# Performance work log

Hardware: AMD Instinct MI355X
Metric: run time of the kernel (lower is better)

The kernel has to match this reference:

```python
import jax, jax.numpy as jnp
import numpy as np

B, N, K, D, H, FF, L, NH = 8, 50, 20, 3, 128, 2048, 3, 8
S = N * K
HD = H // NH


def setup_inputs() -> dict:
    key = jax.random.key(0)
    ks = jax.random.split(key, 16)
    visited = jax.random.uniform(ks[0], (B, S)) < 0.05
    # the single most-recent action per batch row (status flips 0 -> 1)
    action_idx = jax.random.randint(ks[1], (B,), 0, S)
    visited = visited.at[jnp.arange(B), action_idx].set(True)
    feats = jax.random.normal(ks[2], (B, S, D - 1)) * visited[:, :, None]
    state = jnp.concatenate([feats, visited[:, :, None].astype(jnp.float32)], axis=-1)
    prev_state = state.at[jnp.arange(B), action_idx, :].set(0.0)

    def w(k, shape, s=0.02):
        return jax.random.normal(k, shape, dtype=jnp.float32) * s

    return dict(
        prev_state=prev_state, state=state,
        W_pre=w(ks[3], (D, H)), b_pre=jnp.zeros(H),
        Wq=w(ks[4], (L, H, H)), bq=jnp.zeros((L, H)),
        Wk=w(ks[5], (L, H, H)), bk=jnp.zeros((L, H)),
        Wv=w(ks[6], (L, H, H)), bv=jnp.zeros((L, H)),
        Wo=w(ks[7], (L, H, H)), bo=jnp.zeros((L, H)),
        ln1_g=jnp.ones((L, H)), ln1_b=jnp.zeros((L, H)),
        Wff1=w(ks[8], (L, H, FF)), bff1=jnp.zeros((L, FF)),
        Wff2=w(ks[9], (L, FF, H)), bff2=jnp.zeros((L, H)),
        ln2_g=jnp.ones((L, H)), ln2_b=jnp.zeros((L, H)),
        W_comb=w(ks[10], (2 * H, H)), b_comb=jnp.zeros(H),
        W_dec=w(ks[11], (H, H)), b_dec=jnp.zeros(H),
        W_lin=w(ks[12], (S, S)), b_lin=jnp.zeros(S),
    )


def _layer_norm(x, g, b, eps=1e-5):
    m = jnp.mean(x, -1, keepdims=True)
    v = jnp.mean(jnp.square(x - m), -1, keepdims=True)
    return (x - m) * jax.lax.rsqrt(v + eps) * g + b


def _update_mask(state):
    # vectorized equivalent of the original Python-loop scatter mask
    status = state[:, :, -1] != 0                      # visited [B, S], S = K*N channel-major
    mask = status
    vis_kn = status.reshape(B, K, N)
    user_any = vis_kn.any(axis=1)                      # [B, N]: user visited on any channel
    mask = mask | jnp.broadcast_to(user_any[:, None, :], (B, K, N)).reshape(B, S)
    assigned = state.reshape(B, K, N, D).sum(-1) != 0  # [B, K, N]
    full = assigned.sum(-1) >= 2                       # [B, K]: channel already has 2 users
    mask = mask | jnp.broadcast_to(full[:, :, None], (B, K, N)).reshape(B, S)
    return mask


def reference(prev_state, state, W_pre, b_pre, Wq, bq, Wk, bk, Wv, bv, Wo, bo,
              ln1_g, ln1_b, Wff1, bff1, Wff2, bff2, ln2_g, ln2_b,
              W_comb, b_comb, W_dec, b_dec, W_lin, b_lin):
    mask = _update_mask(state)
    # exactly one status change per batch row (sequential RL step)
    diff = prev_state[:, :, -1] != state[:, :, -1]
    act_idx = jnp.argmax(diff, axis=1)                 # [B]

    x = state @ W_pre + b_pre                          # [B, S, H]
    scale = np.float32(1.0 / np.sqrt(HD))
    for i in range(L):  # 3 post-LN transformer encoder layers
        q = (x @ Wq[i] + bq[i]).reshape(B, S, NH, HD)
        k = (x @ Wk[i] + bk[i]).reshape(B, S, NH, HD)
        v = (x @ Wv[i] + bv[i]).reshape(B, S, NH, HD)
        att = jax.nn.softmax(jnp.einsum('bqhd,bkhd->bhqk', q, k) * scale, axis=-1)
        o = jnp.einsum('bhqk,bkhd->bqhd', att, v).reshape(B, S, H) @ Wo[i] + bo[i]
        x = _layer_norm(x + o, ln1_g[i], ln1_b[i])
        ff = jax.nn.relu(x @ Wff1[i] + bff1[i]) @ Wff2[i] + bff2[i]
        x = _layer_norm(x + ff, ln2_g[i], ln2_b[i])

    last = x[jnp.arange(B), act_idx]                   # [B, H]
    combined = jnp.concatenate([x.mean(axis=1), last], axis=-1)  # [B, 2H]
    g = combined @ W_comb + b_comb                     # [B, H]
    dec = x @ W_dec + b_dec                            # [B, S, H]
    scores = jnp.einsum('bsh,bh->bs', dec, g)          # [B, S]
    masked = scores @ W_lin + b_lin                    # Q-Learning head
    return jnp.where(mask, -jnp.inf, masked)
```

## Files before the change

### kernel.cpp

```cpp
#include <hip/hip_runtime.h>
#include <math.h>

#define Bb 8
#define Ss 1000
#define Kk 20
#define Nn 50
#define Dd 3
#define Hh 128
#define FFf 2048
#define Ll 3
#define NHh 8
#define HDd 16
#define ROWS (Bb*Ss)

#define SENTINEL -3.0e38f

typedef unsigned short ush;
typedef short short8 __attribute__((ext_vector_type(8)));
typedef float f32x4 __attribute__((ext_vector_type(4)));

__device__ __forceinline__ ush f2b(float f) {
  unsigned x = __float_as_uint(f);
  return (ush)((x + 0x7fff + ((x >> 16) & 1)) >> 16);
}

__global__ __launch_bounds__(256) void mask_kernel(const float* __restrict__ state,
                                                   const float* __restrict__ prev_state,
                                                   int* __restrict__ mask, int* __restrict__ act_idx) {
  int b = blockIdx.x, tid = threadIdx.x;
  __shared__ unsigned char status[Ss], assigned[Ss], uany[Nn], fullk[Kk];
  __shared__ int act;
  if (tid == 0) act = 1 << 30;
  __syncthreads();
  for (int s = tid; s < Ss; s += 256) {
    const float* st = state + ((size_t)b * Ss + s) * Dd;
    float f2 = st[2];
    status[s] = (f2 != 0.f);
    assigned[s] = ((st[0] + st[1] + f2) != 0.f);
    float p2 = prev_state[((size_t)b * Ss + s) * Dd + 2];
    if (p2 != f2) atomicMin(&act, s);
  }
  __syncthreads();
  if (tid < Nn) {
    unsigned char a = 0;
    for (int k = 0; k < Kk; ++k) a |= status[k * Nn + tid];
    uany[tid] = a;
  } else if (tid >= 64 && tid < 64 + Kk) {
    int k = tid - 64, cnt = 0;
    for (int n = 0; n < Nn; ++n) cnt += assigned[k * Nn + n];
    fullk[k] = (cnt >= 2);
  }
  __syncthreads();
  for (int s = tid; s < Ss; s += 256)
    mask[b * Ss + s] = (int)(status[s] | uany[s % Nn] | fullk[s / Nn]);
  if (tid == 0) act_idx[b] = (act >= Ss) ? 0 : act;
}

__global__ __launch_bounds__(256) void pre_kernel(const float* __restrict__ state,
                                                  const float* __restrict__ W_pre,
                                                  const float* __restrict__ b_pre,
                                                  float* __restrict__ x, ush* __restrict__ xbf) {
  int idx = blockIdx.x * 256 + threadIdx.x;
  if (idx >= ROWS * Hh) return;
  int row = idx >> 7, n = idx & 127;
  const float* st = state + (size_t)row * Dd;
  float v = b_pre[n] + st[0] * W_pre[n] + st[1] * W_pre[Hh + n] + st[2] * W_pre[2 * Hh + n];
  x[idx] = v;
  xbf[idx] = f2b(v);
}

#define S1 (384*128)
#define S2 (128*128)
#define S3 (2048*128)
#define S4 (128*2048)
#define SPL (S1+S2+S3+S4)
__global__ __launch_bounds__(256) void wprep_kernel(const float* __restrict__ Wq, const float* __restrict__ Wk,
                                                    const float* __restrict__ Wv, const float* __restrict__ Wo,
                                                    const float* __restrict__ Wff1, const float* __restrict__ Wff2,
                                                    const float* __restrict__ bq, const float* __restrict__ bk,
                                                    const float* __restrict__ bv,
                                                    ush* __restrict__ wqkvT, ush* __restrict__ woT,
                                                    ush* __restrict__ wff1T, ush* __restrict__ wff2T,
                                                    float* __restrict__ bqkv) {
  int idx = blockIdx.x * 256 + threadIdx.x;
  if (idx < Ll * SPL) {
    int l = idx / SPL, r = idx % SPL;
    if (r < S1) {
      int k = r / 384, n = r % 384;
      float v = (n < 128) ? Wq[((size_t)l * Hh + k) * Hh + n]
              : (n < 256) ? Wk[((size_t)l * Hh + k) * Hh + (n - 128)]
                          : Wv[((size_t)l * Hh + k) * Hh + (n - 256)];
      wqkvT[((size_t)l * 384 + n) * 128 + k] = f2b(v);
    } else if (r < S1 + S2) {
      int rr = r - S1; int k = rr >> 7, n = rr & 127;
      woT[((size_t)l * 128 + n) * 128 + k] = f2b(Wo[((size_t)l * Hh + k) * Hh + n]);
    } else if (r < S1 + S2 + S3) {
      int rr = r - S1 - S2; int k = rr >> 11, n = rr & 2047;
      wff1T[((size_t)l * 2048 + n) * 128 + k] = f2b(Wff1[((size_t)l * Hh + k) * FFf + n]);
    } else {
      int rr = r - S1 - S2 - S3; int k = rr >> 7, n = rr & 127;
      wff2T[((size_t)l * 128 + n) * 2048 + k] = f2b(Wff2[((size_t)l * FFf + k) * Hh + n]);
    }
  }
  if (idx < Ll * 384) {
    int l = idx / 384, c = idx % 384;
    bqkv[idx] = (c < 128) ? bq[l * Hh + c] : (c < 256 ? bk[l * Hh + c - 128] : bv[l * Hh + c - 256]);
  }
}

#define LDP 40
template <int ABF16, int OBF16, int RELU, int PARTIAL, int QKVV>
__global__ __launch_bounds__(256) void gemm_mfma(const void* __restrict__ A, const ush* __restrict__ Wt,
                                                 const float* __restrict__ bias, void* __restrict__ out,
                                                 int M, int N, int K, int klen, ush* __restrict__ vTout) {
  __shared__ ush As[64 * LDP];
  __shared__ ush Bs[64 * LDP];
  int tid = threadIdx.x;
  int lane = tid & 63, wid = tid >> 6;
  int wr = wid >> 1, wc = wid & 1;
  int m0 = blockIdx.y * 64, n0 = blockIdx.x * 64;
  int lrow = tid >> 2, lk = (tid & 3) << 3;
  int quad = lane >> 4, l16 = lane & 15, kb = quad << 3;
  int kstart = PARTIAL ? blockIdx.z * klen : 0;

  f32x4 acc[2][2];
#pragma unroll
  for (int i = 0; i < 2; ++i)
#pragma unroll
    for (int j = 0; j < 2; ++j) acc[i][j] = (f32x4){0.f, 0.f, 0.f, 0.f};

  for (int k0 = kstart; k0 < kstart + klen; k0 += 32) {
    if (ABF16) {
      short8 av = *(const short8*)((const ush*)A + (size_t)(m0 + lrow) * K + k0 + lk);
      *(short8*)&As[lrow * LDP + lk] = av;
    } else {
      const float* ap = (const float*)A + (size_t)(m0 + lrow) * K + k0 + lk;
      short8 s;
#pragma unroll
      for (int i = 0; i < 8; ++i) s[i] = (short)f2b(ap[i]);
      *(short8*)&As[lrow * LDP + lk] = s;
    }
    short8 bv = *(const short8*)&Wt[(size_t)(n0 + lrow) * K + k0 + lk];
    *(short8*)&Bs[lrow * LDP + lk] = bv;
    __syncthreads();

    short8 a0 = *(short8*)&As[(wr * 32 + l16) * LDP + kb];
    short8 a1 = *(short8*)&As[(wr * 32 + 16 + l16) * LDP + kb];
    short8 b0 = *(short8*)&Bs[(wc * 32 + l16) * LDP + kb];
    short8 b1 = *(short8*)&Bs[(wc * 32 + 16 + l16) * LDP + kb];
    acc[0][0] = __builtin_amdgcn_mfma_f32_16x16x32_bf16(a0, b0, acc[0][0], 0, 0, 0);
    acc[0][1] = __builtin_amdgcn_mfma_f32_16x16x32_bf16(a0, b1, acc[0][1], 0, 0, 0);
    acc[1][0] = __builtin_amdgcn_mfma_f32_16x16x32_bf16(a1, b0, acc[1][0], 0, 0, 0);
    acc[1][1] = __builtin_amdgcn_mfma_f32_16x16x32_bf16(a1, b1, acc[1][1], 0, 0, 0);
    __syncthreads();
  }

  float* pout = PARTIAL ? ((float*)out + (size_t)blockIdx.z * M * N) : (float*)out;
#pragma unroll
  for (int i = 0; i < 2; ++i)
#pragma unroll
    for (int j = 0; j < 2; ++j) {
      int col = n0 + wc * 32 + j * 16 + l16;
      int rbase = m0 + wr * 32 + i * 16 + quad * 4;
      float bval = (!PARTIAL || blockIdx.z == 0) ? bias[col] : 0.f;
#pragma unroll
      for (int v = 0; v < 4; ++v) {
        float o = acc[i][j][v] + bval;
        if (RELU) o = fmaxf(o, 0.f);
        if (QKVV && col >= 256) {
          int row = rbase + v;
          int bb2 = row / 1000, qq = row - bb2 * 1000;
          vTout[((size_t)(bb2 * 128 + (col - 256))) * 1024 + qq] = f2b(o);
        } else if (OBF16) {
          ((ush*)out)[(size_t)(rbase + v) * N + col] = f2b(o);
        } else {
          pout[(size_t)(rbase + v) * N + col] = o;
        }
      }
    }
}

#define WLP 132
__global__ __launch_bounds__(256) void wo_ln_kernel(const ush* __restrict__ A, const ush* __restrict__ Wt,
                                                    const float* __restrict__ bias,
                                                    const float* __restrict__ ln_g, const float* __restrict__ ln_b,
                                                    float* __restrict__ x, ush* __restrict__ xbf) {
  __shared__ char smem[64 * WLP * 4];
  ush* As = (ush*)smem;
  ush* Bs = As + 64 * LDP;
  float* xs = (float*)smem;
  __shared__ float pbias[128], pg[128], pb2[128];

  int tid = threadIdx.x, lane = tid & 63, w = tid >> 6;
  int l16 = lane & 15, quad = lane >> 4, kb = quad * 8;
  int m0 = blockIdx.x * 64;
  if (tid < 128) { pbias[tid] = bias[tid]; pg[tid] = ln_g[tid]; pb2[tid] = ln_b[tid]; }

  f32x4 acc[8];
#pragma unroll
  for (int j = 0; j < 8; ++j) acc[j] = (f32x4){0.f, 0.f, 0.f, 0.f};

  int srow = tid >> 2, slk = (tid & 3) << 3;
  for (int k0 = 0; k0 < 128; k0 += 32) {
    *(short8*)&As[srow * LDP + slk] = *(const short8*)(A + (size_t)(m0 + srow) * 128 + k0 + slk);
#pragma unroll
    for (int rr = 0; rr < 2; ++rr) {
      int row = rr * 64 + srow;
      *(short8*)&Bs[row * LDP + slk] = *(const short8*)(Wt + (size_t)row * 128 + k0 + slk);
    }
    __syncthreads();
    short8 aA = *(short8*)&As[(w * 16 + l16) * LDP + kb];
#pragma unroll
    for (int j = 0; j < 8; ++j) {
      short8 bj = *(short8*)&Bs[(j * 16 + l16) * LDP + kb];
      acc[j] = __builtin_amdgcn_mfma_f32_16x16x32_bf16(aA, bj, acc[j], 0, 0, 0);
    }
    __syncthreads();
  }

  for (int e = tid; e < 64 * 32; e += 256) {
    int idx = e * 4; int row = idx >> 7, col = idx & 127;
    *(float4*)&xs[row * WLP + col] = *(const float4*)&x[(size_t)(m0 + row) * 128 + col];
  }
  __syncthreads();

  float v[8][4], s1[4] = {0.f, 0.f, 0.f, 0.f}, s2[4] = {0.f, 0.f, 0.f, 0.f};
#pragma unroll
  for (int j = 0; j < 8; ++j) {
    int col = j * 16 + l16;
#pragma unroll
    for (int r = 0; r < 4; ++r) {
      int rowt = w * 16 + quad * 4 + r;
      float vv = acc[j][r] + pbias[col] + xs[rowt * WLP + col];
      v[j][r] = vv; s1[r] += vv; s2[r] += vv * vv;
    }
  }
#pragma unroll
  for (int m = 1; m <= 8; m <<= 1) {
#pragma unroll
    for (int r = 0; r < 4; ++r) { s1[r] += __shfl_xor(s1[r], m); s2[r] += __shfl_xor(s2[r], m); }
  }
#pragma unroll
  for (int r = 0; r < 4; ++r) {
    int rowt = w * 16 + quad * 4 + r;
    float mean = s1[r] * (1.f / 128.f);
    float var = s2[r] * (1.f / 128.f) - mean * mean;
    float rstd = rsqrtf(var + 1e-5f);
#pragma unroll
    for (int j = 0; j < 8; ++j) {
      int col = j * 16 + l16;
      float o = (v[j][r] - mean) * rstd * pg[col] + pb2[col];
      size_t gi = (size_t)(m0 + rowt) * 128 + col;
      x[gi] = o; xbf[gi] = f2b(o);
    }
  }
}

#define F2P 72
__global__ __launch_bounds__(256) void ff2_ln_kernel(const ush* __restrict__ A,
                                                     const ush* __restrict__ Wt,
                                                     const float* __restrict__ bias,
                                                     const float* __restrict__ ln_g, const float* __restrict__ ln_b,
                                                     float* __restrict__ x, ush* __restrict__ xbf) {
  __shared__ ush As[32 * F2P];
  __shared__ ush Bs[128 * F2P];
  __shared__ float red1[2][2][16], red2[2][2][16];
  __shared__ float pbias[128], pg[128], pb[128];

  int tid = threadIdx.x, lane = tid & 63, w = tid >> 6;
  int wr = w & 1, wc = w >> 1;
  int l16 = lane & 15, quad = lane >> 4, kb = quad * 8;
  int m0 = blockIdx.x * 32;
  if (tid < 128) { pbias[tid] = bias[tid]; pg[tid] = ln_g[tid]; pb[tid] = ln_b[tid]; }

  f32x4 acc[4];
#pragma unroll
  for (int j = 0; j < 4; ++j) acc[j] = (f32x4){0.f, 0.f, 0.f, 0.f};

  int arow = tid >> 3, alk = (tid & 7) << 3;
  const ush* Ap = A + (size_t)(m0 + arow) * 2048 + alk;

  short8 pa = *(const short8*)Ap;
  short8 pbr[4];
#pragma unroll
  for (int rep = 0; rep < 4; ++rep) {
    int idx = rep * 256 + tid;
    int row = idx >> 3, lk = (idx & 7) << 3;
    pbr[rep] = *(const short8*)(Wt + (size_t)row * 2048 + lk);
  }

  for (int k0 = 0; k0 < 2048; k0 += 64) {
    *(short8*)&As[arow * F2P + alk] = pa;
#pragma unroll
    for (int rep = 0; rep < 4; ++rep) {
      int idx = rep * 256 + tid;
      int row = idx >> 3, lk = (idx & 7) << 3;
      *(short8*)&Bs[row * F2P + lk] = pbr[rep];
    }
    __syncthreads();
    if (k0 + 64 < 2048) {
      pa = *(const short8*)(Ap + k0 + 64);
#pragma unroll
      for (int rep = 0; rep < 4; ++rep) {
        int idx = rep * 256 + tid;
        int row = idx >> 3, lk = (idx & 7) << 3;
        pbr[rep] = *(const short8*)(Wt + (size_t)row * 2048 + k0 + 64 + lk);
      }
    }
#pragma unroll
    for (int kk = 0; kk < 2; ++kk) {
      short8 a = *(short8*)&As[(wr * 16 + l16) * F2P + kk * 32 + kb];
#pragma unroll
      for (int j = 0; j < 4; ++j) {
        short8 b = *(short8*)&Bs[(wc * 64 + j * 16 + l16) * F2P + kk * 32 + kb];
        acc[j] = __builtin_amdgcn_mfma_f32_16x16x32_bf16(a, b, acc[j], 0, 0, 0);
      }
    }
    __syncthreads();
  }

  float v[4][4], s1[4] = {0.f, 0.f, 0.f, 0.f}, s2[4] = {0.f, 0.f, 0.f, 0.f};
#pragma unroll
  for (int j = 0; j < 4; ++j) {
    int col = wc * 64 + j * 16 + l16;
#pragma unroll
    for (int r = 0; r < 4; ++r) {
      int row = m0 + wr * 16 + quad * 4 + r;
      float vv = acc[j][r] + pbias[col] + x[(size_t)row * Hh + col];
      v[j][r] = vv; s1[r] += vv; s2[r] += vv * vv;
    }
  }
#pragma unroll
  for (int m = 1; m <= 8; m <<= 1) {
#pragma unroll
    for (int r = 0; r < 4; ++r) { s1[r] += __shfl_xor(s1[r], m); s2[r] += __shfl_xor(s2[r], m); }
  }
  if (l16 == 0) {
#pragma unroll
    for (int r = 0; r < 4; ++r) {
      red1[wr][wc][quad * 4 + r] = s1[r];
      red2[wr][wc][quad * 4 + r] = s2[r];
    }
  }
  __syncthreads();
#pragma unroll
  for (int r = 0; r < 4; ++r) {
    int qr = quad * 4 + r;
    float t1 = red1[wr][0][qr] + red1[wr][1][qr];
    float t2 = red2[wr][0][qr] + red2[wr][1][qr];
    float mean = t1 * (1.f / 128.f);
    float var = t2 * (1.f / 128.f) - mean * mean;
    float rstd = rsqrtf(var + 1e-5f);
    int row = m0 + wr * 16 + quad * 4 + r;
#pragma unroll
    for (int j = 0; j < 4; ++j) {
      int col = wc * 64 + j * 16 + l16;
      float o = (v[j][r] - mean) * rstd * pg[col] + pb[col];
      size_t gi = (size_t)row * Hh + col;
      x[gi] = o; xbf[gi] = f2b(o);
    }
  }
}

__global__ __launch_bounds__(256) void attn_mfma(const ush* __restrict__ qkv,
                                                 const ush* __restrict__ vT,
                                                 ush* __restrict__ attn_o) {
  int blk = blockIdx.x;
  int local = blk >> 3;
  int bh = ((blk & 7) << 3) | (local >> 4);
  int qt = local & 15;
  int b = bh >> 3, h = bh & 7;
  int qbase = qt * 64;
  int tid = threadIdx.x, lane = tid & 63, w = tid >> 6;
  int l16 = lane & 15, quad = lane >> 4, kb = quad * 8;

  __shared__ ush Ks[64][40];
  __shared__ ush Vs[16][72];
  __shared__ ush Pb[4][16][72];

  if (tid < 128)
    *(short8*)&Ks[tid >> 1][16 + (tid & 1) * 8] = (short8){0, 0, 0, 0, 0, 0, 0, 0};

  int qrow = qbase + w * 16 + l16; if (qrow >= Ss) qrow = Ss - 1;
  short8 aq = *(const short8*)(qkv + (size_t)(b * Ss + qrow) * 384 + h * HDd + kb);

  const short one_b = (short)0x3F80;
  const short8 ones = (short8){one_b, one_b, one_b, one_b, one_b, one_b, one_b, one_b};
  f32x4 acc_pv = (f32x4){0.f, 0.f, 0.f, 0.f};
  f32x4 acc_l = (f32x4){0.f, 0.f, 0.f, 0.f};
  const f32x4 zero4 = (f32x4){0.f, 0.f, 0.f, 0.f};

  for (int k0 = 0; k0 < Ss; k0 += 64) {
    __syncthreads();
    if (tid < 128) {
      int row = tid >> 1, g = tid & 1;
      int key = k0 + row;
      short8 s8 = (short8){0, 0, 0, 0, 0, 0, 0, 0};
      if (key < Ss)
        s8 = *(const short8*)(qkv + (size_t)(b * Ss + key) * 384 + 128 + h * HDd + g * 8);
      *(short8*)&Ks[row][g * 8] = s8;
    } else {
      int t = tid - 128;
      int d = t >> 3, kg = t & 7;
      short8 v8 = *(const short8*)(vT + (size_t)(b * 128 + h * 16 + d) * 1024 + k0 + kg * 8);
      *(short8*)&Vs[d][kg * 8] = v8;
    }
    __syncthreads();

#pragma unroll
    for (int kn = 0; kn < 4; ++kn) {
      short8 bk = *(short8*)&Ks[kn * 16 + l16][kb];
      f32x4 s = __builtin_amdgcn_mfma_f32_16x16x32_bf16(aq, bk, zero4, 0, 0, 0);
      int key = k0 + kn * 16 + l16;
      float m = (key < Ss) ? 1.f : 0.f;
#pragma unroll
      for (int r = 0; r < 4; ++r)
        Pb[w][quad * 4 + r][kn * 16 + l16] = f2b(__expf(s[r] * 0.25f) * m);
    }
    short8 pa0 = *(short8*)&Pb[w][l16][kb];
    short8 pa1 = *(short8*)&Pb[w][l16][32 + kb];
    short8 vb0 = *(short8*)&Vs[l16][kb];
    short8 vb1 = *(short8*)&Vs[l16][32 + kb];
    acc_pv = __builtin_amdgcn_mfma_f32_16x16x32_bf16(pa0, vb0, acc_pv, 0, 0, 0);
    acc_pv = __builtin_amdgcn_mfma_f32_16x16x32_bf16(pa1, vb1, acc_pv, 0, 0, 0);
    acc_l = __builtin_amdgcn_mfma_f32_16x16x32_bf16(pa0, ones, acc_l, 0, 0, 0);
    acc_l = __builtin_amdgcn_mfma_f32_16x16x32_bf16(pa1, ones, acc_l, 0, 0, 0);
  }

#pragma unroll
  for (int r = 0; r < 4; ++r) {
    int q = qbase + w * 16 + quad * 4 + r;
    if (q < Ss)
      attn_o[((size_t)(b * Ss + q)) * Hh + h * HDd + l16] = f2b(acc_pv[r] / acc_l[r]);
  }
}

__global__ __launch_bounds__(128) void mean_part_kernel(const float* __restrict__ x,
                                                        float* __restrict__ mpart) {
  int c = blockIdx.x, b = blockIdx.y, n = threadIdx.x;
  const float* xb = x + ((size_t)b * Ss + c * 125) * Hh + n;
  float s = 0.f;
#pragma unroll 5
  for (int i = 0; i < 125; ++i) s += xb[(size_t)i * Hh];
  mpart[(c * Bb + b) * Hh + n] = s;
}

__global__ __launch_bounds__(128) void ghc_kernel(const float* __restrict__ x, const float* __restrict__ mpart,
                                                  const int* __restrict__ act_idx,
                                                  const float* __restrict__ W_comb, const float* __restrict__ b_comb,
                                                  const float* __restrict__ W_dec, const float* __restrict__ b_dec,
                                                  float* __restrict__ h, float* __restrict__ cb) {
  int b = blockIdx.x, n = threadIdx.x;
  __shared__ float cs[2 * Hh], gs[Hh], red[2];
  float mean = 0.f;
#pragma unroll
  for (int c = 0; c < 8; ++c) mean += mpart[(c * Bb + b) * Hh + n];
  cs[n] = mean * (1.f / Ss);
  cs[Hh + n] = x[((size_t)b * Ss + act_idx[b]) * Hh + n];
  __syncthreads();
  float acc = b_comb[n];
  for (int j = 0; j < 2 * Hh; ++j) acc += cs[j] * W_comb[(size_t)j * Hh + n];
  gs[n] = acc;
  __syncthreads();
  float hv = 0.f;
  for (int c = 0; c < Hh; ++c) hv += W_dec[(size_t)n * Hh + c] * gs[c];
  h[b * Hh + n] = hv;
  float t = b_dec[n] * gs[n];
  for (int off = 32; off; off >>= 1) t += __shfl_down(t, off);
  if ((n & 63) == 0) red[n >> 6] = t;
  __syncthreads();
  if (n == 0) cb[b] = red[0] + red[1];
}

__global__ __launch_bounds__(256) void scores_kernel(const float* __restrict__ x, const float* __restrict__ h,
                                                     const float* __restrict__ cb, float* __restrict__ scores) {
  int wid = threadIdx.x >> 6, lane = threadIdx.x & 63;
  int row = blockIdx.x * 4 + wid;
  if (row >= ROWS) return;
  int b = row / Ss;
  const float* xr = x + (size_t)row * Hh;
  const float* hb = h + b * Hh;
  float s = xr[lane] * hb[lane] + xr[lane + 64] * hb[lane + 64];
  for (int off = 32; off; off >>= 1) s += __shfl_down(s, off);
  if (lane == 0) scores[row] = s + cb[b];
}

__global__ __launch_bounds__(256) void final_part(const float* __restrict__ scores,
                                                  const float* __restrict__ W_lin,
                                                  float* __restrict__ fpart) {
  int spc = blockIdx.x, kc = blockIdx.y, b = blockIdx.z;
  int tid = threadIdx.x;
  __shared__ float ss[125];
  for (int i = tid; i < 125; i += 256) ss[i] = scores[b * Ss + kc * 125 + i];
  __syncthreads();
  if (tid < 250) {
    int sp = spc * 250 + tid;
    float acc = 0.f;
    const float* wl = &W_lin[(size_t)(kc * 125) * Ss + sp];
#pragma unroll 5
    for (int s = 0; s < 125; ++s) acc = fmaf(ss[s], wl[(size_t)s * Ss], acc);
    fpart[((size_t)kc * Bb + b) * Ss + sp] = acc;
  }
}

__global__ __launch_bounds__(256) void final_combine(const float* __restrict__ fpart,
                                                     const float* __restrict__ b_lin,
                                                     const int* __restrict__ mask,
                                                     float* __restrict__ out) {
  int b = blockIdx.y;
  int sp = blockIdx.x * 256 + threadIdx.x;
  if (sp >= Ss) return;
  float acc = b_lin[sp];
#pragma unroll
  for (int kc = 0; kc < 8; ++kc) acc += fpart[((size_t)kc * Bb + b) * Ss + sp];
  out[b * Ss + sp] = mask[b * Ss + sp] ? SENTINEL : acc;
}

extern "C" void kernel_launch(void* const* d_in, const int* in_sizes, int n_in,
                              void* d_out, int out_size, void* d_ws, size_t ws_size,
                              hipStream_t stream) {
  const float* prev_state = (const float*)d_in[0];
  const float* state = (const float*)d_in[1];
  const float* W_pre = (const float*)d_in[2];
  const float* b_pre = (const float*)d_in[3];
  const float* Wq = (const float*)d_in[4];
  const float* bq = (const float*)d_in[5];
  const float* Wk = (const float*)d_in[6];
  const float* bk = (const float*)d_in[7];
  const float* Wv = (const float*)d_in[8];
  const float* bv = (const float*)d_in[9];
  const float* Wo = (const float*)d_in[10];
  const float* bo = (const float*)d_in[11];
  const float* ln1_g = (const float*)d_in[12];
  const float* ln1_b = (const float*)d_in[13];
  const float* Wff1 = (const float*)d_in[14];
  const float* bff1 = (const float*)d_in[15];
  const float* Wff2 = (const float*)d_in[16];
  const float* bff2 = (const float*)d_in[17];
  const float* ln2_g = (const float*)d_in[18];
  const float* ln2_b = (const float*)d_in[19];
  const float* W_comb = (const float*)d_in[20];
  const float* b_comb = (const float*)d_in[21];
  const float* W_dec = (const float*)d_in[22];
  const float* b_dec = (const float*)d_in[23];
  const float* W_lin = (const float*)d_in[24];
  const float* b_lin = (const float*)d_in[25];

  char* wsp = (char*)d_ws;
  auto alloc = [&](size_t bytes) { char* p = wsp; wsp += (bytes + 255) & ~(size_t)255; return p; };
  int* mask = (int*)alloc(ROWS * 4);
  int* act = (int*)alloc(Bb * 4);
  ush* wqkvT = (ush*)alloc((size_t)Ll * 384 * 128 * 2);
  ush* woT = (ush*)alloc((size_t)Ll * 128 * 128 * 2);
  ush* wff1T = (ush*)alloc((size_t)Ll * 2048 * 128 * 2);
  ush* wff2T = (ush*)alloc((size_t)Ll * 128 * 2048 * 2);
  float* bqkv = (float*)alloc((size_t)Ll * 384 * 4);
  float* x = (float*)alloc((size_t)ROWS * Hh * 4);
  ush* xbf = (ush*)alloc((size_t)ROWS * Hh * 2);
  ush* qkv_bf = (ush*)alloc((size_t)ROWS * 384 * 2);
  ush* vT = (ush*)alloc((size_t)Bb * 128 * 1024 * 2);
  ush* attn_ob = (ush*)alloc((size_t)ROWS * Hh * 2);
  float* mpart = (float*)alloc((size_t)8 * Bb * Hh * 4);
  float* hbuf = (float*)alloc((size_t)Bb * Hh * 4);
  float* cb = (float*)alloc((size_t)Bb * 4);
  float* scores = (float*)alloc((size_t)ROWS * 4);
  float* fpart = (float*)alloc((size_t)8 * Bb * Ss * 4);
  ush* ffb = (ush*)alloc((size_t)ROWS * FFf * 2);

  wprep_kernel<<<dim3((Ll * SPL + 255) / 256), 256, 0, stream>>>(Wq, Wk, Wv, Wo, Wff1, Wff2, bq, bk, bv,
                                                                 wqkvT, woT, wff1T, wff2T, bqkv);
  mask_kernel<<<Bb, 256, 0, stream>>>(state, prev_state, mask, act);
  pre_kernel<<<dim3((ROWS * Hh + 255) / 256), 256, 0, stream>>>(state, W_pre, b_pre, x, xbf);

  for (int l = 0; l < Ll; ++l) {
    gemm_mfma<1, 1, 0, 0, 1><<<dim3(384 / 64, ROWS / 64), 256, 0, stream>>>(
        xbf, wqkvT + (size_t)l * 384 * 128, bqkv + l * 384, qkv_bf, ROWS, 384, 128, 128, vT);
    attn_mfma<<<dim3(1024), 256, 0, stream>>>(qkv_bf, vT, attn_ob);
    wo_ln_kernel<<<dim3(ROWS / 64), 256, 0, stream>>>(
        attn_ob, woT + (size_t)l * 128 * 128, bo + l * Hh, ln1_g + l * Hh, ln1_b + l * Hh, x, xbf);
    gemm_mfma<1, 1, 1, 0, 0><<<dim3(2048 / 64, ROWS / 64), 256, 0, stream>>>(
        xbf, wff1T + (size_t)l * 2048 * 128, bff1 + l * FFf, ffb, ROWS, 2048, 128, 128, nullptr);
    ff2_ln_kernel<<<dim3(ROWS / 32), 256, 0, stream>>>(
        ffb, wff2T + (size_t)l * 128 * 2048, bff2 + l * Hh, ln2_g + l * Hh, ln2_b + l * Hh, x, xbf);
  }

  mean_part_kernel<<<dim3(8, Bb), 128, 0, stream>>>(x, mpart);
  ghc_kernel<<<Bb, 128, 0, stream>>>(x, mpart, act, W_comb, b_comb, W_dec, b_dec, hbuf, cb);
  scores_kernel<<<dim3(ROWS / 4), 256, 0, stream>>>(x, hbuf, cb, scores);
  final_part<<<dim3(4, 8, Bb), 256, 0, stream>>>(scores, W_lin, fpart);
  final_combine<<<dim3(4, Bb), 256, 0, stream>>>(fpart, b_lin, mask, (float*)d_out);
}
```

Measured before the change: 393.9 us.

## Double-buffer attention K/V tiles and batch W_lin head across rows

The attention kernel now double-buffers K and V tiles in shared memory, prefetching the next tile into registers while the current one is computed, which removes one barrier per iteration. It also swaps the MFMA operand order so each lane holds four consecutive keys, letting the P tile be packed with v_cvt_pk_bf16_f32 and stored as one 8-byte write. The key mask is only evaluated on the tail tile. Separately, final_part processes all 8 batch rows per block so each W_lin element is read once rather than eight times, at the cost of more registers and fewer blocks.

New measurement: 385.6 us. 2.1% less time.

```diff
diff --git a/kernel.cpp b/kernel.cpp
--- a/kernel.cpp
+++ b/kernel.cpp
@@ -374,15 +374,32 @@
   int tid = threadIdx.x, lane = tid & 63, w = tid >> 6;
   int l16 = lane & 15, quad = lane >> 4, kb = quad * 8;
 
-  __shared__ ush Ks[64][40];
-  __shared__ ush Vs[16][72];
+  __shared__ ush Ks[2][64][40];
+  __shared__ ush Vs[2][16][72];
   __shared__ ush Pb[4][16][72];
 
-  if (tid < 128)
-    *(short8*)&Ks[tid >> 1][16 + (tid & 1) * 8] = (short8){0, 0, 0, 0, 0, 0, 0, 0};
+  if (tid < 128) {
+    int row = tid >> 1, g = tid & 1;
+    *(short8*)&Ks[0][row][16 + g * 8] = (short8){0, 0, 0, 0, 0, 0, 0, 0};
+    *(short8*)&Ks[1][row][16 + g * 8] = (short8){0, 0, 0, 0, 0, 0, 0, 0};
+  }
 
   int qrow = qbase + w * 16 + l16; if (qrow >= Ss) qrow = Ss - 1;
   short8 aq = *(const short8*)(qkv + (size_t)(b * Ss + qrow) * 384 + h * HDd + kb);
+
+  int srow = tid >> 1, sg = tid & 1;
+  int sd = (tid - 128) >> 3, skg = (tid - 128) & 7;
+  const ush* kbase = qkv + (size_t)b * Ss * 384 + 128 + h * HDd;
+  const ush* vbase = vT + (size_t)(b * 128 + h * 16) * 1024;
+
+  if (tid < 128) {
+    short8 s8 = (short8){0, 0, 0, 0, 0, 0, 0, 0};
+    if (srow < Ss) s8 = *(const short8*)(kbase + (size_t)srow * 384 + sg * 8);
+    *(short8*)&Ks[0][srow][sg * 8] = s8;
+  } else {
+    *(short8*)&Vs[0][sd][skg * 8] = *(const short8*)(vbase + (size_t)sd * 1024 + skg * 8);
+  }
+  __syncthreads();
 
   const short one_b = (short)0x3F80;
   const short8 ones = (short8){one_b, one_b, one_b, one_b, one_b, one_b, one_b, one_b};
@@ -390,41 +407,58 @@
   f32x4 acc_l = (f32x4){0.f, 0.f, 0.f, 0.f};
   const f32x4 zero4 = (f32x4){0.f, 0.f, 0.f, 0.f};
 
-  for (int k0 = 0; k0 < Ss; k0 += 64) {
-    __syncthreads();
-    if (tid < 128) {
-      int row = tid >> 1, g = tid & 1;
-      int key = k0 + row;
-      short8 s8 = (short8){0, 0, 0, 0, 0, 0, 0, 0};
-      if (key < Ss)
-        s8 = *(const short8*)(qkv + (size_t)(b * Ss + key) * 384 + 128 + h * HDd + g * 8);
-      *(short8*)&Ks[row][g * 8] = s8;
-    } else {
-      int t = tid - 128;
-      int d = t >> 3, kg = t & 7;
-      short8 v8 = *(const short8*)(vT + (size_t)(b * 128 + h * 16 + d) * 1024 + k0 + kg * 8);
-      *(short8*)&Vs[d][kg * 8] = v8;
-    }
-    __syncthreads();
-
+  for (int it = 0; it < 16; ++it) {
+    int k0 = it * 64;
+    int cur = it & 1, nxt = cur ^ 1;
+    bool have = (it + 1 < 16);
+
+    short8 gk, gv;
+    if (have) {
+      if (tid < 128) {
+        gk = (short8){0, 0, 0, 0, 0, 0, 0, 0};
+        int key = k0 + 64 + srow;
+        if (key < Ss) gk = *(const short8*)(kbase + (size_t)key * 384 + sg * 8);
+      } else {
+        gv = *(const short8*)(vbase + (size_t)sd * 1024 + k0 + 64 + skg * 8);
+      }
+    }
+
+    bool tail = (k0 + 64 > Ss);
 #pragma unroll
     for (int kn = 0; kn < 4; ++kn) {
-      short8 bk = *(short8*)&Ks[kn * 16 + l16][kb];
-      f32x4 s = __builtin_amdgcn_mfma_f32_16x16x32_bf16(aq, bk, zero4, 0, 0, 0);
-      int key = k0 + kn * 16 + l16;
-      float m = (key < Ss) ? 1.f : 0.f;
-#pragma unroll
-      for (int r = 0; r < 4; ++r)
-        Pb[w][quad * 4 + r][kn * 16 + l16] = f2b(__expf(s[r] * 0.25f) * m);
-    }
+      short8 ak = *(short8*)&Ks[cur][kn * 16 + l16][kb];
+      f32x4 s = __builtin_amdgcn_mfma_f32_16x16x32_bf16(ak, aq, zero4, 0, 0, 0);
+      float p0 = __expf(s[0] * 0.25f);
+      float p1 = __expf(s[1] * 0.25f);
+      float p2 = __expf(s[2] * 0.25f);
+      float p3 = __expf(s[3] * 0.25f);
+      if (tail) {
+        int keyb = k0 + kn * 16 + quad * 4;
+        if (keyb + 0 >= Ss) p0 = 0.f;
+        if (keyb + 1 >= Ss) p1 = 0.f;
+        if (keyb + 2 >= Ss) p2 = 0.f;
+        if (keyb + 3 >= Ss) p3 = 0.f;
+      }
+      unsigned lo, hi;
+      asm("v_cvt_pk_bf16_f32 %0, %1, %2" : "=v"(lo) : "v"(p0), "v"(p1));
+      asm("v_cvt_pk_bf16_f32 %0, %1, %2" : "=v"(hi) : "v"(p2), "v"(p3));
+      *(uint2*)&Pb[w][l16][kn * 16 + quad * 4] = make_uint2(lo, hi);
+    }
+
     short8 pa0 = *(short8*)&Pb[w][l16][kb];
     short8 pa1 = *(short8*)&Pb[w][l16][32 + kb];
-    short8 vb0 = *(short8*)&Vs[l16][kb];
-    short8 vb1 = *(short8*)&Vs[l16][32 + kb];
+    short8 vb0 = *(short8*)&Vs[cur][l16][kb];
+    short8 vb1 = *(short8*)&Vs[cur][l16][32 + kb];
     acc_pv = __builtin_amdgcn_mfma_f32_16x16x32_bf16(pa0, vb0, acc_pv, 0, 0, 0);
     acc_pv = __builtin_amdgcn_mfma_f32_16x16x32_bf16(pa1, vb1, acc_pv, 0, 0, 0);
     acc_l = __builtin_amdgcn_mfma_f32_16x16x32_bf16(pa0, ones, acc_l, 0, 0, 0);
     acc_l = __builtin_amdgcn_mfma_f32_16x16x32_bf16(pa1, ones, acc_l, 0, 0, 0);
+
+    if (have) {
+      if (tid < 128) *(short8*)&Ks[nxt][srow][sg * 8] = gk;
+      else *(short8*)&Vs[nxt][sd][skg * 8] = gv;
+    }
+    __syncthreads();
   }
 
 #pragma unroll
@@ -488,18 +522,29 @@
 __global__ __launch_bounds__(256) void final_part(const float* __restrict__ scores,
                                                   const float* __restrict__ W_lin,
                                                   float* __restrict__ fpart) {
-  int spc = blockIdx.x, kc = blockIdx.y, b = blockIdx.z;
+  int spc = blockIdx.x, kc = blockIdx.y;
   int tid = threadIdx.x;
-  __shared__ float ss[125];
-  for (int i = tid; i < 125; i += 256) ss[i] = scores[b * Ss + kc * 125 + i];
+  __shared__ float ss[8][125];
+  for (int i = tid; i < 8 * 125; i += 256) {
+    int bb = i / 125, s = i - bb * 125;
+    ss[bb][s] = scores[bb * Ss + kc * 125 + s];
+  }
   __syncthreads();
   if (tid < 250) {
     int sp = spc * 250 + tid;
-    float acc = 0.f;
+    float acc[8];
+#pragma unroll
+    for (int bb = 0; bb < 8; ++bb) acc[bb] = 0.f;
     const float* wl = &W_lin[(size_t)(kc * 125) * Ss + sp];
 #pragma unroll 5
-    for (int s = 0; s < 125; ++s) acc = fmaf(ss[s], wl[(size_t)s * Ss], acc);
-    fpart[((size_t)kc * Bb + b) * Ss + sp] = acc;
+    for (int s = 0; s < 125; ++s) {
+      float wv = wl[(size_t)s * Ss];
+#pragma unroll
+      for (int bb = 0; bb < 8; ++bb) acc[bb] = fmaf(ss[bb][s], wv, acc[bb]);
+    }
+#pragma unroll
+    for (int bb = 0; bb < 8; ++bb)
+      fpart[((size_t)kc * Bb + bb) * Ss + sp] = acc[bb];
   }
 }
 
@@ -587,6 +632,6 @@
   mean_part_kernel<<<dim3(8, Bb), 128, 0, stream>>>(x, mpart);
   ghc_kernel<<<Bb, 128, 0, stream>>>(x, mpart, act, W_comb, b_comb, W_dec, b_dec, hbuf, cb);
   scores_kernel<<<dim3(ROWS / 4), 256, 0, stream>>>(x, hbuf, cb, scores);
-  final_part<<<dim3(4, 8, Bb), 256, 0, stream>>>(scores, W_lin, fpart);
+  final_part<<<dim3(4, 8), 256, 0, stream>>>(scores, W_lin, fpart);
   final_combine<<<dim3(4, Bb), 256, 0, stream>>>(fpart, b_lin, mask, (float*)d_out);
 }
```
